# Kernel tuning notes

Measured on AMD Instinct MI355X. Metric: run time of the kernel, lower is better.

## Reference

```python
import jax, jax.numpy as jnp
import numpy as np

K_HOPS = 2  # SGConv K = nlayers


def setup_inputs() -> dict:
    key = jax.random.key(0)
    k1, k2, k3 = jax.random.split(key, 3)
    N, E, F, C = 100000, 1600000, 128, 40
    x = jax.random.normal(k1, (N, F), dtype=jnp.float32)
    edge_index = jax.random.randint(k2, (2, E), 0, N, dtype=jnp.int64)
    W = jax.random.normal(k3, (C, F), dtype=jnp.float32) * (1.0 / np.sqrt(F))
    b = jnp.zeros((C,), dtype=jnp.float32)
    return {"x": x, "edge_index": edge_index, "W": W, "b": b}


def reference(x, edge_index, W, b):
    # SGConv: K hops of GCN-normalized propagation (with self-loops), then Linear.
    N = x.shape[0]
    loop = jnp.arange(N, dtype=edge_index.dtype)
    src = jnp.concatenate([edge_index[0], loop])  # message source
    dst = jnp.concatenate([edge_index[1], loop])  # aggregation target
    w = jnp.ones(src.shape[0], dtype=x.dtype)     # edge_weight=None -> 1, self-loop fill=1
    deg = jax.ops.segment_sum(w, dst, num_segments=N)  # in-degree incl. self-loop (>=1)
    dinv = jax.lax.rsqrt(deg)
    norm = dinv[src] * w * dinv[dst]              # D^{-1/2} A D^{-1/2}
    h = x
    for _ in range(K_HOPS):
        h = jax.ops.segment_sum(norm[:, None] * h[src], dst, num_segments=N)
    return h @ W.T + b
```

## Files before the change

kernel.cpp:

```cpp
#include <hip/hip_runtime.h>
#include <hip/hip_fp16.h>
#include <cstdint>

#define CDIM 40
#define FDIM 128
#define BIN_SHIFT 8
#define BIN_SZ (1 << BIN_SHIFT)
#define CHUNK 4096
#define STAGE_CAP 8192

typedef _Float16 f16x8 __attribute__((ext_vector_type(8)));
typedef float f32x4 __attribute__((ext_vector_type(4)));

static __device__ __forceinline__ long long load_idx(const void* p, int is64, long long i) {
    if (is64) return ((const long long*)p)[i];
    return (long long)((const int*)p)[i];
}

static __device__ __forceinline__ unsigned packh2(float a, float b) {
    __half2 h;
    h.x = __float2half(a);
    h.y = __float2half(b);
    return *(unsigned*)&h;
}

static __device__ __forceinline__ void addv2(float* acc, uint2 v) {
    const __half2* h = (const __half2*)&v;
    float2 f0 = __half22float2(h[0]);
    float2 f1 = __half22float2(h[1]);
    acc[0] += f0.x; acc[1] += f0.y; acc[2] += f1.x; acc[3] += f1.y;
}

static __device__ __forceinline__ f16x8 cvt8(float4 a, float4 b) {
    f16x8 r;
    r[0] = (_Float16)a.x; r[1] = (_Float16)a.y; r[2] = (_Float16)a.z; r[3] = (_Float16)a.w;
    r[4] = (_Float16)b.x; r[5] = (_Float16)b.y; r[6] = (_Float16)b.z; r[7] = (_Float16)b.w;
    return r;
}

__global__ void k_init(int* cursor, int nb, int capRec) {
    int i = blockIdx.x * blockDim.x + threadIdx.x;
    if (i < nb) cursor[i] = i * capRec;
}

__global__ __launch_bounds__(256) void kA3(const void* ei, long long E,
                                           int nb, int* __restrict__ cursor,
                                           unsigned* __restrict__ binned) {
    __shared__ unsigned lval[CHUNK];
    __shared__ unsigned short lbin[CHUNK];
    __shared__ int lcnt[512];
    __shared__ int lbase[512];
    __shared__ int lflag;
    int tid = threadIdx.x;
    if (tid == 0) lflag = 1;
    for (int i = tid; i < nb; i += 256) lcnt[i] = 0;
    __syncthreads();
    {
        const unsigned* w = (const unsigned*)ei;
        int nscan = (int)((2 * E < 4096) ? (2 * E) : 4096);
        for (int k = 1 + 2 * tid; k < nscan; k += 512)
            if (w[k] != 0u) lflag = 0;
    }
    __syncthreads();
    int is64 = lflag;
    long long base = (long long)blockIdx.x * CHUNK;
    int nk = (int)min((long long)CHUNK, E - base);
    for (int k = tid; k < nk; k += 256) {
        long long e = base + k;
        int s = (int)load_idx(ei, is64, e);
        int d = (int)load_idx(ei, is64, E + e);
        int bin = d >> BIN_SHIFT;
        lval[k] = (unsigned)s | ((unsigned)(d & (BIN_SZ - 1)) << 17);
        lbin[k] = (unsigned short)bin;
        atomicAdd(&lcnt[bin], 1);
    }
    __syncthreads();
    for (int i = tid; i < nb; i += 256) {
        int c = lcnt[i];
        lbase[i] = c ? atomicAdd(&cursor[i], c) : 0;
        lcnt[i] = 0;
    }
    __syncthreads();
    for (int k = tid; k < nk; k += 256) {
        int bin = lbin[k];
        int loc = atomicAdd(&lcnt[bin], 1);
        binned[lbase[bin] + loc] = lval[k];
    }
}

__global__ __launch_bounds__(256) void kB(const unsigned* __restrict__ binned,
                                          const int* __restrict__ cursor,
                                          int capRec, int capC,
                                          int2* __restrict__ meta,
                                          float* __restrict__ dinv,
                                          int* __restrict__ cursorG,
                                          int* __restrict__ csr, int N) {
    __shared__ int lcnt[BIN_SZ];
    __shared__ int lexcl[BIN_SZ];
    __shared__ int ls[256];
    __shared__ int dh[64];
    __shared__ int tot;
    __shared__ int stage[STAGE_CAP];
    int b = blockIdx.x, tid = threadIdx.x;
    int node0 = b << BIN_SHIFT;
    int nn = min(BIN_SZ, N - node0);
    int recBase = b * capRec;
    int csrBase = b * capC;
    int nedges = cursor[b] - recBase;

    lcnt[tid] = 0;
    if (tid < 64) dh[tid] = 0;
    __syncthreads();
    for (int t = tid; t < nedges; t += 256)
        atomicAdd(&lcnt[(binned[recBase + t] >> 17) & (BIN_SZ - 1)], 1);
    __syncthreads();
    int myc = lcnt[tid];
    int psz = (myc + 3) & ~3;
    ls[tid] = psz;
    __syncthreads();
    for (int off = 1; off < 256; off <<= 1) {
        int t = (tid >= off) ? ls[tid - off] : 0;
        __syncthreads();
        ls[tid] += t;
        __syncthreads();
    }
    int ex = ls[tid] - psz;
    lexcl[tid] = ex;
    if (tid == 255) tot = ls[255];
    if (tid < nn) {
        dinv[node0 + tid] = rsqrtf(1.0f + (float)myc);
        atomicAdd(&dh[min(myc, 63)], 1);
    }
    __syncthreads();
    int total = tot;
    int dv = (tid < 64) ? dh[tid] : 0;
    ls[tid] = dv;
    __syncthreads();
    for (int off = 1; off < 64; off <<= 1) {
        int t = (tid >= off) ? ls[tid - off] : 0;
        __syncthreads();
        ls[tid] += t;
        __syncthreads();
    }
    if (tid < 64) dh[tid] = ls[tid] - dv;
    __syncthreads();
    if (tid < nn) {
        int pos = atomicAdd(&dh[min(myc, 63)], 1);
        int2 mi;
        mi.x = csrBase + ex;
        mi.y = (node0 + tid) | (myc << 17);
        meta[node0 + pos] = mi;
    }
    __syncthreads();
    lcnt[tid] = ex;
    __syncthreads();
    if (total <= STAGE_CAP) {
        for (int t = tid; t < total; t += 256) stage[t] = N;
        __syncthreads();
        for (int t = tid; t < nedges; t += 256) {
            unsigned v = binned[recBase + t];
            int src = (int)(v & 0x1FFFFu);
            int dl  = (int)((v >> 17) & (BIN_SZ - 1));
            int p = atomicAdd(&lcnt[dl], 1);
            stage[p] = src;
        }
        __syncthreads();
        const int4* sp = (const int4*)stage;
        int4* cp = (int4*)(csr + csrBase);
        for (int t = tid; t < (total >> 2); t += 256) cp[t] = sp[t];
    } else {
        if (tid < nn) cursorG[node0 + tid] = csrBase + ex;
        __syncthreads();
        for (int t = tid; t < nedges; t += 256) {
            unsigned v = binned[recBase + t];
            int src = (int)(v & 0x1FFFFu);
            int dl  = (int)((v >> 17) & (BIN_SZ - 1));
            int p = atomicAdd(&cursorG[node0 + dl], 1);
            csr[p] = src;
        }
        if (tid < nn)
            for (int k = myc; k < psz; ++k) csr[csrBase + ex + k] = N;
    }
}

__global__ __launch_bounds__(256) void k_gemm(const float* __restrict__ x,
                                              const float* __restrict__ W,
                                              const float* __restrict__ dinv,
                                              __half* __restrict__ gA,
                                              __half* __restrict__ gB, int N) {
    if (blockIdx.x == 0 && threadIdx.x < 20) {
        if (threadIdx.x < 16) ((unsigned*)(gA + (size_t)N * 32))[threadIdx.x] = 0u;
        else                  ((unsigned*)(gB + (size_t)N * 8))[threadIdx.x - 16] = 0u;
    }
    int wave = threadIdx.x >> 6;
    int lane = threadIdx.x & 63;
    int m = lane & 15;
    int quad = lane >> 4;
    f16x8 bfrag[3][4];
#pragma unroll
    for (int t = 0; t < 3; ++t) {
        int c = t * 16 + m;
#pragma unroll
        for (int q = 0; q < 4; ++q) {
            if (c < CDIM) {
                const float* wp = W + (size_t)c * FDIM + q * 32 + quad * 8;
                float4 w0 = *(const float4*)wp;
                float4 w1 = *(const float4*)(wp + 4);
                bfrag[t][q] = cvt8(w0, w1);
            } else {
                f16x8 z = {0, 0, 0, 0, 0, 0, 0, 0};
                bfrag[t][q] = z;
            }
        }
    }
#pragma unroll
    for (int i = 0; i < 4; ++i) {
        int nodebase = blockIdx.x * 256 + wave * 64 + i * 16;
        if (nodebase >= N) break;
        const float* xp = x + (size_t)(nodebase + m) * FDIM + quad * 8;
        f16x8 afrag[4];
#pragma unroll
        for (int q = 0; q < 4; ++q) {
            float4 x0 = *(const float4*)(xp + q * 32);
            float4 x1 = *(const float4*)(xp + q * 32 + 4);
            afrag[q] = cvt8(x0, x1);
        }
        f32x4 acc0 = {0, 0, 0, 0}, acc1 = {0, 0, 0, 0}, acc2 = {0, 0, 0, 0};
#pragma unroll
        for (int q = 0; q < 4; ++q) {
            acc0 = __builtin_amdgcn_mfma_f32_16x16x32_f16(afrag[q], bfrag[0][q], acc0, 0, 0, 0);
            acc1 = __builtin_amdgcn_mfma_f32_16x16x32_f16(afrag[q], bfrag[1][q], acc1, 0, 0, 0);
            acc2 = __builtin_amdgcn_mfma_f32_16x16x32_f16(afrag[q], bfrag[2][q], acc2, 0, 0, 0);
        }
        float4 dvv = *(const float4*)&dinv[nodebase + quad * 4];
        float ds[4] = {dvv.x, dvv.y, dvv.z, dvv.w};
#pragma unroll
        for (int r = 0; r < 4; ++r) {
            int node = nodebase + quad * 4 + r;
            gA[(size_t)node * 32 + m]      = __float2half(acc0[r] * ds[r]);
            gA[(size_t)node * 32 + 16 + m] = __float2half(acc1[r] * ds[r]);
            if (m < 8)
                gB[(size_t)node * 8 + m]   = __float2half(acc2[r] * ds[r]);
        }
    }
}

__global__ __launch_bounds__(256) void k_gather(const int2* __restrict__ meta,
                                                const int* __restrict__ csr,
                                                const __half* __restrict__ gA,
                                                const __half* __restrict__ gB,
                                                const float* __restrict__ b,
                                                __half* __restrict__ goA,
                                                __half* __restrict__ goB,
                                                float* __restrict__ outF,
                                                int N, int mode) {
    unsigned t = blockIdx.x * 256 + threadIdx.x;
    if (mode == 0 && t < 20) {
        if (t < 16) ((unsigned*)(goA + (size_t)N * 32))[t] = 0u;
        else        ((unsigned*)(goB + (size_t)N * 8))[t - 16] = 0u;
    }
    unsigned gidx = t / 10, c = t - gidx * 10;
    if (gidx >= (unsigned)N) return;
    int2 mi = meta[gidx];
    int j = mi.x;
    int node = mi.y & 0x1FFFF;
    int deg = mi.y >> 17;
    int end_pad = j + ((deg + 3) & ~3);
    const uint2* src;
    unsigned stride;
    if (c < 8) { src = (const uint2*)gA + c;       stride = 8; }
    else       { src = (const uint2*)gB + (c - 8); stride = 2; }
    float acc[4] = {0.0f, 0.0f, 0.0f, 0.0f};
    addv2(acc, src[(size_t)node * stride]);
    for (; j + 8 <= end_pad; j += 8) {
        int4 c0 = *(const int4*)&csr[j];
        int4 c1 = *(const int4*)&csr[j + 4];
        uint2 v0 = src[(size_t)c0.x * stride];
        uint2 v1 = src[(size_t)c0.y * stride];
        uint2 v2 = src[(size_t)c0.z * stride];
        uint2 v3 = src[(size_t)c0.w * stride];
        uint2 v4 = src[(size_t)c1.x * stride];
        uint2 v5 = src[(size_t)c1.y * stride];
        uint2 v6 = src[(size_t)c1.z * stride];
        uint2 v7 = src[(size_t)c1.w * stride];
        addv2(acc, v0); addv2(acc, v1); addv2(acc, v2); addv2(acc, v3);
        addv2(acc, v4); addv2(acc, v5); addv2(acc, v6); addv2(acc, v7);
    }
    if (j < end_pad) {
        int4 c0 = *(const int4*)&csr[j];
        uint2 v0 = src[(size_t)c0.x * stride];
        uint2 v1 = src[(size_t)c0.y * stride];
        uint2 v2 = src[(size_t)c0.z * stride];
        uint2 v3 = src[(size_t)c0.w * stride];
        addv2(acc, v0); addv2(acc, v1); addv2(acc, v2); addv2(acc, v3);
    }
    float d = rsqrtf(1.0f + (float)deg);
    if (mode == 0) {
        float s = d * d;
        uint2 o;
        o.x = packh2(acc[0] * s, acc[1] * s);
        o.y = packh2(acc[2] * s, acc[3] * s);
        if (c < 8) ((uint2*)goA)[(size_t)node * 8 + c] = o;
        else       ((uint2*)goB)[(size_t)node * 2 + (c - 8)] = o;
    } else {
        float4 bv = ((const float4*)b)[c];
        float4 o;
        o.x = acc[0] * d + bv.x;
        o.y = acc[1] * d + bv.y;
        o.z = acc[2] * d + bv.z;
        o.w = acc[3] * d + bv.w;
        ((float4*)outF)[(size_t)node * 10 + c] = o;
    }
}

static inline size_t align256(size_t v) { return (v + 255) & ~(size_t)255; }

extern "C" void kernel_launch(void* const* d_in, const int* in_sizes, int n_in,
                              void* d_out, int out_size, void* d_ws, size_t ws_size,
                              hipStream_t stream) {
    const float* x  = (const float*)d_in[0];
    const void*  ei = d_in[1];
    const float* W  = (const float*)d_in[2];
    const float* b  = (const float*)d_in[3];
    float* out = (float*)d_out;

    const int N = in_sizes[0] / FDIM;
    const long long E = (long long)in_sizes[1] / 2;

    const int nb     = (N + BIN_SZ - 1) >> BIN_SHIFT;
    const int nchunk = (int)((E + CHUNK - 1) / CHUNK);
    int capRec = (int)(E / nb) + 2048;
    if (capRec > STAGE_CAP) capRec = STAGE_CAP;
    int capC = (capRec + BIN_SZ * 3 + 1027) & ~3;

    char* wsb = (char*)d_ws;
    size_t off = 0;
    int*      cursor  = (int*)(wsb + off);      off = align256(off + (size_t)nb * 4);
    int*      cursorG = (int*)(wsb + off);      off = align256(off + (size_t)N * 4);
    int2*     meta    = (int2*)(wsb + off);     off = align256(off + (size_t)N * 8);
    float*    dinv    = (float*)(wsb + off);    off = align256(off + (size_t)N * 4);
    __half*   gA0     = (__half*)(wsb + off);   off = align256(off + (size_t)(N + 1) * 32 * 2);
    __half*   gB0     = (__half*)(wsb + off);   off = align256(off + (size_t)(N + 1) * 8 * 2);
    __half*   gA1     = (__half*)(wsb + off);   off = align256(off + (size_t)(N + 1) * 32 * 2);
    __half*   gB1     = (__half*)(wsb + off);   off = align256(off + (size_t)(N + 1) * 8 * 2);
    unsigned* binned  = (unsigned*)(wsb + off); off = align256(off + (size_t)nb * capRec * 4);
    int*      csr     = (int*)(wsb + off);      off = align256(off + (size_t)nb * capC * 4);

    const int B = 256;
    const int nbGE = (N + 255) / 256;
    const unsigned GT = 10u * (unsigned)N;
    const int nbGA = (int)((GT + B - 1) / B);

    k_init  <<<(nb + 255) / 256, 256, 0, stream>>>(cursor, nb, capRec);
    kA3     <<<nchunk, B, 0, stream>>>(ei, E, nb, cursor, binned);
    kB      <<<nb, B, 0, stream>>>(binned, cursor, capRec, capC, meta, dinv, cursorG, csr, N);
    k_gemm  <<<nbGE, B, 0, stream>>>(x, W, dinv, gA0, gB0, N);
    k_gather<<<nbGA, B, 0, stream>>>(meta, csr, gA0, gB0, b, gA1, gB1, nullptr, N, 0);
    k_gather<<<nbGA, B, 0, stream>>>(meta, csr, gA1, gB1, b, nullptr, nullptr, out, N, 1);
}
```

Baseline: 213.4 us.

## Replicate bin cursors four ways and double edge chunk size in binning

```diff
diff --git a/kernel.cpp b/kernel.cpp
--- a/kernel.cpp
+++ b/kernel.cpp
@@ -6,7 +6,8 @@
 #define FDIM 128
 #define BIN_SHIFT 8
 #define BIN_SZ (1 << BIN_SHIFT)
-#define CHUNK 4096
+#define CHUNK 8192
+#define RREP 4
 #define STAGE_CAP 8192
 
 typedef _Float16 f16x8 __attribute__((ext_vector_type(8)));
@@ -38,9 +39,12 @@
     return r;
 }
 
-__global__ void k_init(int* cursor, int nb, int capRec) {
+__global__ void k_init(int* cursor, int nb, int capRec, int subCap) {
     int i = blockIdx.x * blockDim.x + threadIdx.x;
-    if (i < nb) cursor[i] = i * capRec;
+    if (i < RREP * nb) {
+        int r = i / nb, b = i - r * nb;
+        cursor[i] = b * capRec + r * subCap;
+    }
 }
 
 __global__ __launch_bounds__(256) void kA3(const void* ei, long long E,
@@ -52,6 +56,7 @@
     __shared__ int lbase[512];
     __shared__ int lflag;
     int tid = threadIdx.x;
+    int rep = blockIdx.x & (RREP - 1);
     if (tid == 0) lflag = 1;
     for (int i = tid; i < nb; i += 256) lcnt[i] = 0;
     __syncthreads();
@@ -77,7 +82,7 @@
     __syncthreads();
     for (int i = tid; i < nb; i += 256) {
         int c = lcnt[i];
-        lbase[i] = c ? atomicAdd(&cursor[i], c) : 0;
+        lbase[i] = c ? atomicAdd(&cursor[rep * nb + i], c) : 0;
         lcnt[i] = 0;
     }
     __syncthreads();
@@ -90,11 +95,11 @@
 
 __global__ __launch_bounds__(256) void kB(const unsigned* __restrict__ binned,
                                           const int* __restrict__ cursor,
-                                          int capRec, int capC,
+                                          int capRec, int subCap, int capC,
                                           int2* __restrict__ meta,
                                           float* __restrict__ dinv,
                                           int* __restrict__ cursorG,
-                                          int* __restrict__ csr, int N) {
+                                          int* __restrict__ csr, int N, int nb) {
     __shared__ int lcnt[BIN_SZ];
     __shared__ int lexcl[BIN_SZ];
     __shared__ int ls[256];
@@ -104,15 +109,22 @@
     int b = blockIdx.x, tid = threadIdx.x;
     int node0 = b << BIN_SHIFT;
     int nn = min(BIN_SZ, N - node0);
-    int recBase = b * capRec;
     int csrBase = b * capC;
-    int nedges = cursor[b] - recBase;
+    int starts[RREP], cnts[RREP];
+#pragma unroll
+    for (int r = 0; r < RREP; ++r) {
+        int st = b * capRec + r * subCap;
+        starts[r] = st;
+        cnts[r] = cursor[r * nb + b] - st;
+    }
 
     lcnt[tid] = 0;
     if (tid < 64) dh[tid] = 0;
     __syncthreads();
-    for (int t = tid; t < nedges; t += 256)
-        atomicAdd(&lcnt[(binned[recBase + t] >> 17) & (BIN_SZ - 1)], 1);
+#pragma unroll
+    for (int r = 0; r < RREP; ++r)
+        for (int t = tid; t < cnts[r]; t += 256)
+            atomicAdd(&lcnt[(binned[starts[r] + t] >> 17) & (BIN_SZ - 1)], 1);
     __syncthreads();
     int myc = lcnt[tid];
     int psz = (myc + 3) & ~3;
@@ -157,13 +169,15 @@
     if (total <= STAGE_CAP) {
         for (int t = tid; t < total; t += 256) stage[t] = N;
         __syncthreads();
-        for (int t = tid; t < nedges; t += 256) {
-            unsigned v = binned[recBase + t];
-            int src = (int)(v & 0x1FFFFu);
-            int dl  = (int)((v >> 17) & (BIN_SZ - 1));
-            int p = atomicAdd(&lcnt[dl], 1);
-            stage[p] = src;
-        }
+#pragma unroll
+        for (int r = 0; r < RREP; ++r)
+            for (int t = tid; t < cnts[r]; t += 256) {
+                unsigned v = binned[starts[r] + t];
+                int src = (int)(v & 0x1FFFFu);
+                int dl  = (int)((v >> 17) & (BIN_SZ - 1));
+                int p = atomicAdd(&lcnt[dl], 1);
+                stage[p] = src;
+            }
         __syncthreads();
         const int4* sp = (const int4*)stage;
         int4* cp = (int4*)(csr + csrBase);
@@ -171,15 +185,19 @@
     } else {
         if (tid < nn) cursorG[node0 + tid] = csrBase + ex;
         __syncthreads();
-        for (int t = tid; t < nedges; t += 256) {
-            unsigned v = binned[recBase + t];
-            int src = (int)(v & 0x1FFFFu);
-            int dl  = (int)((v >> 17) & (BIN_SZ - 1));
-            int p = atomicAdd(&cursorG[node0 + dl], 1);
-            csr[p] = src;
-        }
-        if (tid < nn)
-            for (int k = myc; k < psz; ++k) csr[csrBase + ex + k] = N;
+#pragma unroll
+        for (int r = 0; r < RREP; ++r)
+            for (int t = tid; t < cnts[r]; t += 256) {
+                unsigned v = binned[starts[r] + t];
+                int src = (int)(v & 0x1FFFFu);
+                int dl  = (int)((v >> 17) & (BIN_SZ - 1));
+                int p = atomicAdd(&cursorG[node0 + dl], 1);
+                csr[p] = src;
+            }
+        if (tid < nn) {
+            int st = csrBase + ex;
+            for (int k = myc; k < psz; ++k) csr[st + k] = N;
+        }
     }
 }
 
@@ -329,13 +347,14 @@
 
     const int nb     = (N + BIN_SZ - 1) >> BIN_SHIFT;
     const int nchunk = (int)((E + CHUNK - 1) / CHUNK);
-    int capRec = (int)(E / nb) + 2048;
-    if (capRec > STAGE_CAP) capRec = STAGE_CAP;
+    int subCap = ((int)(E / nb) / RREP + 512 + 3) & ~3;
+    int capRec = subCap * RREP;
+    if (capRec > 2 * STAGE_CAP) capRec = 2 * STAGE_CAP;
     int capC = (capRec + BIN_SZ * 3 + 1027) & ~3;
 
     char* wsb = (char*)d_ws;
     size_t off = 0;
-    int*      cursor  = (int*)(wsb + off);      off = align256(off + (size_t)nb * 4);
+    int*      cursor  = (int*)(wsb + off);      off = align256(off + (size_t)RREP * nb * 4);
     int*      cursorG = (int*)(wsb + off);      off = align256(off + (size_t)N * 4);
     int2*     meta    = (int2*)(wsb + off);     off = align256(off + (size_t)N * 8);
     float*    dinv    = (float*)(wsb + off);    off = align256(off + (size_t)N * 4);
@@ -351,9 +370,10 @@
     const unsigned GT = 10u * (unsigned)N;
     const int nbGA = (int)((GT + B - 1) / B);
 
-    k_init  <<<(nb + 255) / 256, 256, 0, stream>>>(cursor, nb, capRec);
+    k_init  <<<(RREP * nb + 255) / 256, 256, 0, stream>>>(cursor, nb, capRec, subCap);
     kA3     <<<nchunk, B, 0, stream>>>(ei, E, nb, cursor, binned);
-    kB      <<<nb, B, 0, stream>>>(binned, cursor, capRec, capC, meta, dinv, cursorG, csr, N);
+    kB      <<<nb, B, 0, stream>>>(binned, cursor, capRec, subCap, capC, meta, dinv,
+                                   cursorG, csr, N, nb);
     k_gemm  <<<nbGE, B, 0, stream>>>(x, W, dinv, gA0, gB0, N);
     k_gather<<<nbGA, B, 0, stream>>>(meta, csr, gA0, gB0, b, gA1, gB1, nullptr, N, 0);
     k_gather<<<nbGA, B, 0, stream>>>(meta, csr, gA1, gB1, b, nullptr, nullptr, out, N, 1);
```

New measurement: 215.2 us. Within noise of the previous version (+0.8%).
